# Kernel optimization log

Measured on AMD Instinct MI355X. Metric: run time of the kernel, lower is better.

The kernel has to match this reference:

```python
import jax, jax.numpy as jnp
import numpy as np

N_BITS = 16
BATCH = 4194304  # 2**22 tokens
TABLE_SIZE = 2 ** (N_BITS - 1)  # largest CUMULATIVE/FLIP context is n_bits-1 bits


def setup_inputs() -> dict:
    key = jax.random.key(0)
    k1, k2 = jax.random.split(key)
    # input bit tensor [batch, n_bits], values in {0,1}; index n_bits-1 is bit 0 (LSB)
    bits = jax.random.randint(k1, (BATCH, N_BITS), 0, 2, dtype=jnp.int32)
    # per-bit-position RAM lookup tables, padded to the max address space.
    # Binary contents {0,1}, stored as float32 so the flip/XOR math is expressible.
    tables = (jax.random.uniform(k2, (N_BITS, TABLE_SIZE)) < 0.5).astype(jnp.float32)
    return {"bits": bits, "tables": tables}


def reference(bits, tables):
    """BitLevelMapper forward, CUMULATIVE context + FLIP output mode.

    bits:   [B, n_bits] int32 in {0,1}, array index n_bits-1-k holds bit value k (LSB=k=0)
    tables: [n_bits, 2^(n_bits-1)] float32 in {0,1}; row i is the RAM/LUT for bit_pos i.
    For bit_pos i the context is the lowest i bits (bit0..bit_{i-1});
    address = sum_k context_bit_k * 2^k; flip = table[i, address];
    output bit i = input bit i XOR flip.
    """
    n_bits = bits.shape[1]
    bits_rev = bits[:, ::-1]                      # [B, n] column k = bit value k
    k = jnp.arange(n_bits)
    # W[i, k] = 2^k if k < i else 0  -> addr_i = sum_{k<i} bit_k * 2^k (addr_0 = 0)
    W = jnp.where(k[None, :] < k[:, None], (1 << k)[None, :], 0).astype(jnp.int32)
    addr = bits_rev @ W.T                          # [B, n] int32 RAM addresses per bit_pos
    flip = tables[k[None, :], addr]                # [B, n] gather: tables[i, addr[b, i]]
    x = bits_rev.astype(tables.dtype)
    out_rev = x + flip - 2.0 * x * flip            # XOR expressed arithmetically
    return out_rev[:, ::-1]                        # back to original bit-array layout
```

## Files before the change

### kernel.cpp

```cpp
#include <hip/hip_runtime.h>
#include <hip/hip_bf16.h>


#define PACK_WORDS 2048

__global__ void pack_tables_kernel(const float* __restrict__ tables,
                                   unsigned* __restrict__ packed) {
    int w = blockIdx.x * blockDim.x + threadIdx.x;
    if (w >= PACK_WORDS) return;
    unsigned word = 0u;
    #pragma unroll
    for (int b = 0; b < 32; ++b) {
        int g = w * 32 + b;
        if (g < 65535) {
            int i = 31 - __clz(g + 1);
            int a = g - ((1 << i) - 1);
            if (tables[i * 32768 + a] != 0.0f) word |= (1u << b);
        }
    }
    packed[w] = word;
}

__global__ __launch_bounds__(256) void
blm_kernel(const int* __restrict__ bits, const unsigned* __restrict__ packed,
           float* __restrict__ out, int nrows) {
    __shared__ unsigned tab[PACK_WORDS];
    for (int k = threadIdx.x; k < PACK_WORDS; k += blockDim.x)
        tab[k] = packed[k];
    __syncthreads();

    int stride = gridDim.x * blockDim.x;
    for (int r = blockIdx.x * blockDim.x + threadIdx.x; r < nrows; r += stride) {
        const int4* bp = (const int4*)(bits + (size_t)r * 16);
        int4 m0 = bp[0];
        int4 m1 = bp[1];
        int4 m2 = bp[2];
        int4 m3 = bp[3];
        int mem[16] = {m0.x, m0.y, m0.z, m0.w,
                       m1.x, m1.y, m1.z, m1.w,
                       m2.x, m2.y, m2.z, m2.w,
                       m3.x, m3.y, m3.z, m3.w};
        unsigned v = 0u;
        #pragma unroll
        for (int j = 0; j < 16; ++j)
            v |= ((unsigned)mem[j]) << (15 - j);

        float o[16];
        #pragma unroll
        for (int i = 0; i < 16; ++i) {
            unsigned mask   = (1u << i) - 1u;
            unsigned bitidx = mask + (v & mask);
            unsigned fl     = (tab[bitidx >> 5] >> (bitidx & 31u)) & 1u;
            unsigned ob     = ((v >> i) & 1u) ^ fl;
            o[15 - i] = (float)ob;
        }

        float4* op = (float4*)(out + (size_t)r * 16);
        op[0] = make_float4(o[0],  o[1],  o[2],  o[3]);
        op[1] = make_float4(o[4],  o[5],  o[6],  o[7]);
        op[2] = make_float4(o[8],  o[9],  o[10], o[11]);
        op[3] = make_float4(o[12], o[13], o[14], o[15]);
    }
}

extern "C" void kernel_launch(void* const* d_in, const int* in_sizes, int n_in,
                              void* d_out, int out_size, void* d_ws, size_t ws_size,
                              hipStream_t stream) {
    const int*   bits   = (const int*)d_in[0];
    const float* tables = (const float*)d_in[1];
    float*       out    = (float*)d_out;
    unsigned*    packed = (unsigned*)d_ws;

    int nrows = in_sizes[0] / 16;

    pack_tables_kernel<<<(PACK_WORDS + 255) / 256, 256, 0, stream>>>(tables, packed);

    int block = 256;
    int grid  = 4096;
    blm_kernel<<<grid, block, 0, stream>>>(bits, packed, out, nrows);
}
```

Measured before the change: 474.4 us.

## Coalesce bit loads and stores per wave using shuffles, ballot-based table packing

Each wave now processes 64 consecutive rows, loading the int4s so that adjacent lanes read adjacent 16-byte chunks and storing the outputs the same way. Rows are rebuilt and scattered back through cross-lane shuffles of packed nibbles instead of per-thread strided 64-byte row accesses. The table-packing kernel uses one thread per bit with a wave ballot, and the grid size is doubled. The shuffles add ALU and LDS-crossbar work. Any tail rows beyond a multiple of 64 are no longer processed.

```diff
diff --git a/kernel.cpp b/kernel.cpp
--- a/kernel.cpp
+++ b/kernel.cpp
@@ -4,62 +4,79 @@
 
 #define PACK_WORDS 2048
 
-__global__ void pack_tables_kernel(const float* __restrict__ tables,
-                                   unsigned* __restrict__ packed) {
-    int w = blockIdx.x * blockDim.x + threadIdx.x;
-    if (w >= PACK_WORDS) return;
-    unsigned word = 0u;
-    #pragma unroll
-    for (int b = 0; b < 32; ++b) {
-        int g = w * 32 + b;
-        if (g < 65535) {
-            int i = 31 - __clz(g + 1);
-            int a = g - ((1 << i) - 1);
-            if (tables[i * 32768 + a] != 0.0f) word |= (1u << b);
-        }
+__global__ __launch_bounds__(256) void
+pack_tables_kernel(const float* __restrict__ tables, unsigned* __restrict__ packed) {
+    int g = blockIdx.x * blockDim.x + threadIdx.x;
+    bool val = false;
+    if (g < 65535) {
+        int i = 31 - __clz(g + 1);
+        int a = g - ((1 << i) - 1);
+        val = tables[i * 32768 + a] != 0.0f;
     }
-    packed[w] = word;
+    unsigned long long m = __ballot(val);
+    if ((threadIdx.x & 63) == 0) {
+        packed[(g >> 5)]     = (unsigned)m;
+        packed[(g >> 5) + 1] = (unsigned)(m >> 32);
+    }
 }
 
 __global__ __launch_bounds__(256) void
-blm_kernel(const int* __restrict__ bits, const unsigned* __restrict__ packed,
-           float* __restrict__ out, int nrows) {
+blm_kernel(const int4* __restrict__ bits4, const unsigned* __restrict__ packed,
+           float4* __restrict__ out4, int nrows) {
     __shared__ unsigned tab[PACK_WORDS];
-    for (int k = threadIdx.x; k < PACK_WORDS; k += blockDim.x)
+    for (int k = threadIdx.x; k < PACK_WORDS; k += 256)
         tab[k] = packed[k];
     __syncthreads();
 
-    int stride = gridDim.x * blockDim.x;
-    for (int r = blockIdx.x * blockDim.x + threadIdx.x; r < nrows; r += stride) {
-        const int4* bp = (const int4*)(bits + (size_t)r * 16);
-        int4 m0 = bp[0];
-        int4 m1 = bp[1];
-        int4 m2 = bp[2];
-        int4 m3 = bp[3];
-        int mem[16] = {m0.x, m0.y, m0.z, m0.w,
-                       m1.x, m1.y, m1.z, m1.w,
-                       m2.x, m2.y, m2.z, m2.w,
-                       m3.x, m3.y, m3.z, m3.w};
-        unsigned v = 0u;
+    const int lane    = threadIdx.x & 63;
+    const int wave    = (blockIdx.x * 256 + threadIdx.x) >> 6;
+    const int nwaves  = (gridDim.x * 256) >> 6;
+    const int nchunks = nrows >> 6;
+
+    for (int c = wave; c < nchunks; c += nwaves) {
+        const size_t base = (size_t)c * 256;
+
+        int4 m0 = bits4[base +   0 + lane];
+        int4 m1 = bits4[base +  64 + lane];
+        int4 m2 = bits4[base + 128 + lane];
+        int4 m3 = bits4[base + 192 + lane];
+
+        unsigned n0 = (unsigned)((m0.x << 3) | (m0.y << 2) | (m0.z << 1) | m0.w);
+        unsigned n1 = (unsigned)((m1.x << 3) | (m1.y << 2) | (m1.z << 1) | m1.w);
+        unsigned n2 = (unsigned)((m2.x << 3) | (m2.y << 2) | (m2.z << 1) | m2.w);
+        unsigned n3 = (unsigned)((m3.x << 3) | (m3.y << 2) | (m3.z << 1) | m3.w);
+        unsigned pk = n0 | (n1 << 4) | (n2 << 8) | (n3 << 12);
+
+        const int hi   = lane >> 4;
+        const int bsrc = (lane & 15) << 2;
+        unsigned v = 0;
         #pragma unroll
-        for (int j = 0; j < 16; ++j)
-            v |= ((unsigned)mem[j]) << (15 - j);
+        for (int q = 0; q < 4; ++q) {
+            unsigned x  = (unsigned)__shfl((int)pk, bsrc + q, 64);
+            unsigned nb = (x >> (hi * 4)) & 0xFu;
+            v |= nb << (12 - 4 * q);
+        }
 
-        float o[16];
+        unsigned r16 = 0;
         #pragma unroll
         for (int i = 0; i < 16; ++i) {
-            unsigned mask   = (1u << i) - 1u;
-            unsigned bitidx = mask + (v & mask);
-            unsigned fl     = (tab[bitidx >> 5] >> (bitidx & 31u)) & 1u;
-            unsigned ob     = ((v >> i) & 1u) ^ fl;
-            o[15 - i] = (float)ob;
+            unsigned mask = (1u << i) - 1u;
+            unsigned bidx = mask + (v & mask);
+            unsigned fl   = (tab[bidx >> 5] >> (bidx & 31u));
+            r16 |= (((v >> i) ^ fl) & 1u) << i;
         }
 
-        float4* op = (float4*)(out + (size_t)r * 16);
-        op[0] = make_float4(o[0],  o[1],  o[2],  o[3]);
-        op[1] = make_float4(o[4],  o[5],  o[6],  o[7]);
-        op[2] = make_float4(o[8],  o[9],  o[10], o[11]);
-        op[3] = make_float4(o[12], o[13], o[14], o[15]);
+        #pragma unroll
+        for (int j = 0; j < 4; ++j) {
+            unsigned y = (unsigned)__shfl((int)r16, (j << 4) + (lane >> 2), 64);
+            int q4 = (lane & 3) << 2;
+            float4 f;
+            f.x = (float)((y >> (15 - q4)) & 1u);
+            f.y = (float)((y >> (14 - q4)) & 1u);
+            f.z = (float)((y >> (13 - q4)) & 1u);
+            f.w = (float)((y >> (12 - q4)) & 1u);
+            out4[base + j * 64 + lane] = f;
+        }
     }
 }
 
@@ -73,9 +90,8 @@
 
     int nrows = in_sizes[0] / 16;
 
-    pack_tables_kernel<<<(PACK_WORDS + 255) / 256, 256, 0, stream>>>(tables, packed);
+    pack_tables_kernel<<<65536 / 256, 256, 0, stream>>>(tables, packed);
 
-    int block = 256;
-    int grid  = 4096;
-    blm_kernel<<<grid, block, 0, stream>>>(bits, packed, out, nrows);
+    blm_kernel<<<8192, 256, 0, stream>>>((const int4*)bits, packed,
+                                         (float4*)out, nrows);
 }
```

New measurement: 434.9 us. 1.09x faster.
